# Kernel optimization log

Measured on AMD Instinct MI355X. Metric: run time of the kernel, lower is better.

## Reference

```python
import jax, jax.numpy as jnp
import numpy as np

DIM = 512
K = 64          # num_clusters
GHOST = 1
ALPHA = 100.0
EPS = 1e-12


def _l2norm(v, axis):
    return v / jnp.maximum(jnp.linalg.norm(v, axis=axis, keepdims=True), EPS)


def setup_inputs() -> dict:
    key = jax.random.key(0)
    k_x, k_c = jax.random.split(key)
    x = jax.random.normal(k_x, (64, DIM, 32, 32), dtype=jnp.float32)
    # centroids ~ orthogonal init in torch; random normal rows, unit-ish scale
    centroids = jax.random.normal(k_c, (K + GHOST, DIM), dtype=jnp.float32) / np.sqrt(DIM)
    conv_w = 2.0 * ALPHA * centroids            # [K+g, C] (1x1 conv kernel squeezed)
    conv_b = -ALPHA * jnp.linalg.norm(centroids, axis=1)  # [K+g]
    return {"x": x, "centroids": centroids, "conv_w": conv_w, "conv_b": conv_b}


def reference(x, centroids, conv_w, conv_b):
    N, C, H, W = x.shape
    L = H * W
    # descriptor-wise L2 normalization over channel dim
    xn = _l2norm(x, axis=1)
    xf = xn.reshape(N, C, L)                                   # [N, C, L]
    # 1x1 conv == per-location matmul; softmax over clusters
    logits = jnp.einsum('kc,ncl->nkl', conv_w, xf) + conv_b[None, :, None]
    a = jax.nn.softmax(logits, axis=1)                         # [N, K+g, L]
    # vlad[n,k,c] = sum_l a[n,k,l]*(x[n,c,l]-cent[k,c])
    #            = (a @ x^T) - (sum_l a) * cent   -- avoids NxKxCxL tensor
    weighted = jnp.einsum('nkl,ncl->nkc', a, xf)               # [N, K+g, C]
    a_sum = jnp.sum(a, axis=-1)                                # [N, K+g]
    vlad = weighted - a_sum[:, :, None] * centroids[None]      # [N, K+g, C]
    vlad = vlad[:, :K, :]                                      # drop ghost clusters
    vlad = _l2norm(vlad, axis=2)                               # intra-normalization
    vlad = vlad.reshape(N, K * C)
    vlad = _l2norm(vlad, axis=1)                               # global L2
    return vlad
```

## Files before the change

kernel.cpp:

```cpp
#include <hip/hip_runtime.h>
#include <hip/hip_bf16.h>

#define C_DIM 512
#define L_DIM 1024
#define KK 64
#define KG 65
#define KP 80

using f32x4  = __attribute__((ext_vector_type(4))) float;
using bf16x8 = __attribute__((ext_vector_type(8))) short;

union U4 { uint4 u; bf16x8 b; };

__device__ __forceinline__ unsigned bfh(float x) { return __float_as_uint(x) >> 16; }
__device__ __forceinline__ float bfh_f(float x) { return __uint_as_float(__float_as_uint(x) & 0xFFFF0000u); }

__device__ __forceinline__ unsigned pack2(float a, float b) {
    return __builtin_amdgcn_perm(__float_as_uint(b), __float_as_uint(a), 0x07060302u);
}

__device__ __forceinline__ void load_lds16(const void* g, void* l) {
    __builtin_amdgcn_global_load_lds(
        (const __attribute__((address_space(1))) void*)g,
        (__attribute__((address_space(3))) void*)l, 16, 0, 0);
}

__global__ void k_prep(const float* __restrict__ conv_w, const float* __restrict__ conv_b,
                       unsigned short* __restrict__ wp, float* __restrict__ wb)
{
    int ch = blockIdx.x;
    int kt = blockIdx.y;
    int t  = threadIdx.x;
    for (int p = 0; p < 2; ++p) {
        int idx = p * 256 + t;
        int lane = idx >> 3, j = idx & 7;
        int k = kt * 16 + (lane & 15);
        int c = ch * 32 + (lane >> 4) * 8 + j;
        float v = (k < KG) ? conv_w[k * C_DIM + c] : 0.f;
        unsigned h = bfh(v);
        float r = v - __uint_as_float(h << 16);
        wp[((ch * 10 + kt) << 9) + idx]     = (unsigned short)h;
        wp[((ch * 10 + 5 + kt) << 9) + idx] = (unsigned short)bfh(r);
    }
    if (ch == 0 && kt == 0 && t < KP) wb[t] = (t < KG) ? conv_b[t] : -1e30f;
}

__global__ __launch_bounds__(256) void k_s1(
    const float* __restrict__ x, const unsigned short* __restrict__ wp,
    const float* __restrict__ wb,
    unsigned* __restrict__ aPh32, unsigned* __restrict__ aPl32,
    float* __restrict__ asum_part)
{
    __shared__ unsigned short wlds[2][10 << 9];

    const int lb = blockIdx.x, n = blockIdx.y;
    const int t = threadIdx.x, lane = t & 63, w = t >> 6;
    const int arow = lane & 15;
    const int agrp = lane >> 4;
    const int lw0 = lb * 128 + w * 32;
    const int choff = (lb + n) & 15;

    const float* xbase = x + (size_t)n * C_DIM * L_DIM;

#define WSTAGE(b, ch) { _Pragma("unroll") \
    for (int i = 0; i < 3; ++i) { \
        int s = w + (i << 2); \
        if (s < 10) { \
            const unsigned short* src = &wp[(((ch) * 10 + s) << 9) + (lane << 3)]; \
            load_lds16(src, &wlds[b][s << 9]); \
        } } }

    f32x4 acc[5][2];
#pragma unroll
    for (int a = 0; a < 5; ++a)
#pragma unroll
        for (int b = 0; b < 2; ++b) acc[a][b] = (f32x4)0.f;
    float ss0 = 0.f, ss1 = 0.f;

    WSTAGE(0, choff)
    asm volatile("s_waitcnt vmcnt(0)" ::: "memory");
    __syncthreads();

#pragma unroll 2
    for (int ch0 = 0; ch0 < 16; ++ch0) {
        const int cur = ch0 & 1;
        const int ch = (ch0 + choff) & 15;
        const int c0 = ch * 32;
        if (ch0 < 15) WSTAGE(cur ^ 1, (ch0 + 1 + choff) & 15)
        float e0[8], e1[8];
#pragma unroll
        for (int j = 0; j < 8; ++j) {
            float2 v = *reinterpret_cast<const float2*>(
                &xbase[(size_t)(c0 + agrp * 8 + j) * L_DIM + lw0 + 2 * arow]);
            e0[j] = v.x;
            e1[j] = v.y;
        }
#pragma unroll
        for (int j = 0; j < 8; ++j) { ss0 += e0[j] * e0[j]; ss1 += e1[j] * e1[j]; }
        U4 bh[2], bl[2];
        bh[0].u.x = pack2(e0[0], e0[1]); bh[0].u.y = pack2(e0[2], e0[3]);
        bh[0].u.z = pack2(e0[4], e0[5]); bh[0].u.w = pack2(e0[6], e0[7]);
        bh[1].u.x = pack2(e1[0], e1[1]); bh[1].u.y = pack2(e1[2], e1[3]);
        bh[1].u.z = pack2(e1[4], e1[5]); bh[1].u.w = pack2(e1[6], e1[7]);
        float r0, r1, r2, r3;
        r0 = e0[0] - bfh_f(e0[0]); r1 = e0[1] - bfh_f(e0[1]);
        r2 = e0[2] - bfh_f(e0[2]); r3 = e0[3] - bfh_f(e0[3]);
        bl[0].u.x = pack2(r0, r1); bl[0].u.y = pack2(r2, r3);
        r0 = e0[4] - bfh_f(e0[4]); r1 = e0[5] - bfh_f(e0[5]);
        r2 = e0[6] - bfh_f(e0[6]); r3 = e0[7] - bfh_f(e0[7]);
        bl[0].u.z = pack2(r0, r1); bl[0].u.w = pack2(r2, r3);
        r0 = e1[0] - bfh_f(e1[0]); r1 = e1[1] - bfh_f(e1[1]);
        r2 = e1[2] - bfh_f(e1[2]); r3 = e1[3] - bfh_f(e1[3]);
        bl[1].u.x = pack2(r0, r1); bl[1].u.y = pack2(r2, r3);
        r0 = e1[4] - bfh_f(e1[4]); r1 = e1[5] - bfh_f(e1[5]);
        r2 = e1[6] - bfh_f(e1[6]); r3 = e1[7] - bfh_f(e1[7]);
        bl[1].u.z = pack2(r0, r1); bl[1].u.w = pack2(r2, r3);
        U4 ah[5], al[5];
#pragma unroll
        for (int kt = 0; kt < 5; ++kt) {
            ah[kt].u = *reinterpret_cast<const uint4*>(&wlds[cur][(kt << 9) + (lane << 3)]);
            al[kt].u = *reinterpret_cast<const uint4*>(&wlds[cur][((5 + kt) << 9) + (lane << 3)]);
        }
#pragma unroll
        for (int kt = 0; kt < 5; ++kt)
#pragma unroll
            for (int lt = 0; lt < 2; ++lt) {
                acc[kt][lt] = __builtin_amdgcn_mfma_f32_16x16x32_bf16(ah[kt].b, bh[lt].b, acc[kt][lt], 0, 0, 0);
                acc[kt][lt] = __builtin_amdgcn_mfma_f32_16x16x32_bf16(ah[kt].b, bl[lt].b, acc[kt][lt], 0, 0, 0);
                acc[kt][lt] = __builtin_amdgcn_mfma_f32_16x16x32_bf16(al[kt].b, bh[lt].b, acc[kt][lt], 0, 0, 0);
            }
        asm volatile("s_waitcnt vmcnt(0)" ::: "memory");
        __syncthreads();
    }

    ss0 += __shfl_xor(ss0, 16, 64); ss0 += __shfl_xor(ss0, 32, 64);
    ss1 += __shfl_xor(ss1, 16, 64); ss1 += __shfl_xor(ss1, 32, 64);
    float invc[2];
    invc[0] = 1.0f / fmaxf(sqrtf(ss0), 1e-12f);
    invc[1] = 1.0f / fmaxf(sqrtf(ss1), 1e-12f);

    float4 wbv[5];
#pragma unroll
    for (int kt = 0; kt < 5; ++kt)
        wbv[kt] = *reinterpret_cast<const float4*>(&wb[kt * 16 + agrp * 4]);

    float aval[5][2][4];
    float rs[2];
#pragma unroll
    for (int lt = 0; lt < 2; ++lt) {
        float m = -1e30f;
#pragma unroll
        for (int kt = 0; kt < 5; ++kt)
#pragma unroll
            for (int r = 0; r < 4; ++r) {
                float lg = acc[kt][lt][r] * invc[lt] + ((const float*)&wbv[kt])[r];
                aval[kt][lt][r] = lg;
                m = fmaxf(m, lg);
            }
        m = fmaxf(m, __shfl_xor(m, 16, 64));
        m = fmaxf(m, __shfl_xor(m, 32, 64));
        float s = 0.f;
#pragma unroll
        for (int kt = 0; kt < 5; ++kt)
#pragma unroll
            for (int r = 0; r < 4; ++r) {
                float e = __expf(aval[kt][lt][r] - m);
                aval[kt][lt][r] = e;
                s += e;
            }
        s += __shfl_xor(s, 16, 64);
        s += __shfl_xor(s, 32, 64);
        rs[lt] = 1.0f / s;
    }

#pragma unroll
    for (int kt = 0; kt < 4; ++kt)
#pragma unroll
        for (int r = 0; r < 4; ++r) {
            int k = kt * 16 + agrp * 4 + r;
            float s01 = 0.f;
#pragma unroll
            for (int lt = 0; lt < 2; ++lt) {
                float a = aval[kt][lt][r] * rs[lt];
                aval[kt][lt][r] = a;
                s01 += a;
            }
#pragma unroll
            for (int off = 8; off; off >>= 1) s01 += __shfl_xor(s01, off, 64);
            if ((lane & 15) == 0)
                asum_part[((n * 8 + lb) * 4 + w) * KK + k] = s01;
            float ap0 = aval[kt][0][r] * invc[0];
            float ap1 = aval[kt][1][r] * invc[1];
            unsigned h0 = bfh(ap0), h1 = bfh(ap1);
            float q0 = ap0 - __uint_as_float(h0 << 16);
            float q1 = ap1 - __uint_as_float(h1 << 16);
            int widx = (n * KK + k) * (L_DIM / 2) + (lw0 >> 1) + arow;
            aPh32[widx] = h0 | (h1 << 16);
            aPl32[widx] = bfh(q0) | (bfh(q1) << 16);
        }
}

__global__ void k_asum(const float* __restrict__ part, float* __restrict__ a_sum)
{
    int id = blockIdx.x * 256 + threadIdx.x;
    int n = id >> 6, k = id & 63;
    float s = 0.f;
#pragma unroll
    for (int p = 0; p < 32; ++p) s += part[(n * 32 + p) * KK + k];
    a_sum[id] = s;
}

#define S2P 72
__global__ __launch_bounds__(256) void k_s2v(
    const float* __restrict__ x, const unsigned short* __restrict__ aPh,
    const unsigned short* __restrict__ aPl, const float* __restrict__ a_sum,
    const float* __restrict__ cent, float* __restrict__ vlad,
    float* __restrict__ rnpart)
{
    __shared__ unsigned short Ah[64 * S2P], Al[64 * S2P];
    __shared__ unsigned short Bh[64 * S2P], Bl[64 * S2P];
    __shared__ float rnbuf[4][64];

    const int flat = blockIdx.x;
    const int cq = flat >> 6;
    const int n  = ((flat & 7) << 3) | ((flat >> 3) & 7);
    const int t = threadIdx.x, lane = t & 63, w = t >> 6;
    const int arow = lane & 15, agrp = lane >> 4;

    f32x4 acc[4];
#pragma unroll
    for (int a = 0; a < 4; ++a) acc[a] = (f32x4)0.f;

    for (int step = 0; step < 16; ++step) {
        const int l0 = step * 64;
        __syncthreads();
#pragma unroll
        for (int p = 0; p < 2; ++p) {
            int idx = p * 256 + t;
            int k = idx >> 3;
            int lc = (idx & 7) * 8;
            size_t g = (size_t)(n * KK + k) * L_DIM + l0 + lc;
            *reinterpret_cast<uint4*>(&Ah[k * S2P + lc]) = *reinterpret_cast<const uint4*>(&aPh[g]);
            *reinterpret_cast<uint4*>(&Al[k * S2P + lc]) = *reinterpret_cast<const uint4*>(&aPl[g]);
        }
#pragma unroll
        for (int p = 0; p < 4; ++p) {
            int idx = p * 256 + t;
            int c = idx >> 4;
            int lc = (idx & 15) * 4;
            float4 v = *reinterpret_cast<const float4*>(
                &x[((size_t)n * C_DIM + cq * 64 + c) * L_DIM + l0 + lc]);
            uint2 hw, lw;
            hw.x = pack2(v.x, v.y); hw.y = pack2(v.z, v.w);
            float r0 = v.x - bfh_f(v.x), r1 = v.y - bfh_f(v.y);
            float r2 = v.z - bfh_f(v.z), r3 = v.w - bfh_f(v.w);
            lw.x = pack2(r0, r1); lw.y = pack2(r2, r3);
            *reinterpret_cast<uint2*>(&Bh[c * S2P + lc]) = hw;
            *reinterpret_cast<uint2*>(&Bl[c * S2P + lc]) = lw;
        }
        __syncthreads();
#pragma unroll
        for (int ks = 0; ks < 2; ++ks) {
            const int koff = ks * 32 + agrp * 8;
            U4 bh, bl;
            bh.u = *reinterpret_cast<const uint4*>(&Bh[(w * 16 + arow) * S2P + koff]);
            bl.u = *reinterpret_cast<const uint4*>(&Bl[(w * 16 + arow) * S2P + koff]);
#pragma unroll
            for (int kt = 0; kt < 4; ++kt) {
                U4 ah, al;
                ah.u = *reinterpret_cast<const uint4*>(&Ah[(kt * 16 + arow) * S2P + koff]);
                al.u = *reinterpret_cast<const uint4*>(&Al[(kt * 16 + arow) * S2P + koff]);
                acc[kt] = __builtin_amdgcn_mfma_f32_16x16x32_bf16(ah.b, bh.b, acc[kt], 0, 0, 0);
                acc[kt] = __builtin_amdgcn_mfma_f32_16x16x32_bf16(ah.b, bl.b, acc[kt], 0, 0, 0);
                acc[kt] = __builtin_amdgcn_mfma_f32_16x16x32_bf16(al.b, bh.b, acc[kt], 0, 0, 0);
            }
        }
    }
    const int c = cq * 64 + w * 16 + arow;
    float myrn[4][4];
#pragma unroll
    for (int kt = 0; kt < 4; ++kt)
#pragma unroll
        for (int r = 0; r < 4; ++r) {
            int k = kt * 16 + agrp * 4 + r;
            float as = a_sum[n * 64 + k];
            float cv = cent[k * C_DIM + c];
            float v = acc[kt][r] - as * cv;
            vlad[((size_t)n * KK + k) * C_DIM + c] = v;
            float sq = v * v;
            sq += __shfl_xor(sq, 1, 64);
            sq += __shfl_xor(sq, 2, 64);
            sq += __shfl_xor(sq, 4, 64);
            sq += __shfl_xor(sq, 8, 64);
            myrn[kt][r] = sq;
        }
    if (arow == 0) {
#pragma unroll
        for (int kt = 0; kt < 4; ++kt)
#pragma unroll
            for (int r = 0; r < 4; ++r)
                rnbuf[w][kt * 16 + agrp * 4 + r] = myrn[kt][r];
    }
    __syncthreads();
    if (t < 64) {
        float s = rnbuf[0][t] + rnbuf[1][t] + rnbuf[2][t] + rnbuf[3][t];
        rnpart[((size_t)n * 64 + t) * 8 + cq] = s;
    }
}

__global__ void k_scale(const float* __restrict__ rnpart, float* __restrict__ scale)
{
    int n = blockIdx.x;
    int k = threadIdx.x;
    float s = 0.f;
#pragma unroll
    for (int q = 0; q < 8; ++q) s += rnpart[((size_t)n * 64 + k) * 8 + q];
    float nrm = sqrtf(s);
    float den = fmaxf(nrm, 1e-12f);
    float tk = nrm / den;
    float tot = tk * tk;
#pragma unroll
    for (int off = 32; off; off >>= 1) tot += __shfl_down(tot, off, 64);
    tot = __shfl(tot, 0, 64);
    float g = fmaxf(sqrtf(tot), 1e-12f);
    scale[n * 64 + k] = 1.0f / (den * g);
}

__global__ void k_out(const float* __restrict__ vlad, const float* __restrict__ scale,
                      float* __restrict__ out)
{
    int nk = blockIdx.x;
    int t = threadIdx.x;
    float sc = scale[nk];
    for (int c = t; c < C_DIM; c += 256)
        out[(size_t)nk * C_DIM + c] = vlad[(size_t)nk * C_DIM + c] * sc;
}

extern "C" void kernel_launch(void* const* d_in, const int* in_sizes, int n_in,
                              void* d_out, int out_size, void* d_ws, size_t ws_size,
                              hipStream_t stream)
{
    const float* x    = (const float*)d_in[0];
    const float* cent = (const float*)d_in[1];
    const float* cw   = (const float*)d_in[2];
    const float* cb   = (const float*)d_in[3];
    float* out = (float*)d_out;
    char* ws = (char*)d_ws;

    unsigned short* wp  = (unsigned short*)(ws + 0);
    float*          wb  = (float*)(ws + 262144);
    unsigned short* aPh = (unsigned short*)(ws + 524288);
    unsigned short* aPl = (unsigned short*)(ws + 8912896);
    float* asum_part    = (float*)(ws + 17301504);
    float* a_sum        = (float*)(ws + 17825792);
    float* vlad         = (float*)(ws + 18874368);
    float* rnpart       = (float*)(ws + 27262976);
    float* scale        = (float*)(ws + 27394048);

    k_prep<<<dim3(16, 5), 256, 0, stream>>>(cw, cb, wp, wb);
    k_s1<<<dim3(8, 64), 256, 0, stream>>>(x, wp, wb,
                                          (unsigned*)aPh, (unsigned*)aPl, asum_part);
    k_asum<<<16, 256, 0, stream>>>(asum_part, a_sum);
    k_s2v<<<512, 256, 0, stream>>>(x, aPh, aPl, a_sum, cent, vlad, rnpart);
    k_scale<<<64, 64, 0, stream>>>(rnpart, scale);
    k_out<<<4096, 256, 0, stream>>>(vlad, scale, out);
}
```

Baseline: 74.44 us.

## Stage x tiles through LDS with async two-deep prefetch and counted waits

Activation tiles are now loaded with global_load_lds into a double-buffered, padded LDS array alongside the weight tiles, prefetching two channel chunks ahead. The full vmcnt(0) drain at the end of each iteration is replaced by per-wave counted waits (vmcnt 6 or 7) followed by a barrier, so the next chunk's loads stay in flight during MFMA work. This targets the exposed global-load latency of the strided float2 x reads in the main loop. In exchange it uses more LDS, which may lower occupancy, and relies on exact per-wave load counts for correctness.

```diff
diff --git a/kernel.cpp b/kernel.cpp
--- a/kernel.cpp
+++ b/kernel.cpp
@@ -45,30 +45,39 @@
     if (ch == 0 && kt == 0 && t < KP) wb[t] = (t < KG) ? conv_b[t] : -1e30f;
 }
 
+#define XSEG 260
 __global__ __launch_bounds__(256) void k_s1(
     const float* __restrict__ x, const unsigned short* __restrict__ wp,
     const float* __restrict__ wb,
     unsigned* __restrict__ aPh32, unsigned* __restrict__ aPl32,
     float* __restrict__ asum_part)
 {
+    __shared__ float xs[2][16 * XSEG];
     __shared__ unsigned short wlds[2][10 << 9];
 
     const int lb = blockIdx.x, n = blockIdx.y;
     const int t = threadIdx.x, lane = t & 63, w = t >> 6;
     const int arow = lane & 15;
     const int agrp = lane >> 4;
-    const int lw0 = lb * 128 + w * 32;
+    const int gl0 = lb * 128;
+    const int lw0 = gl0 + w * 32;
     const int choff = (lb + n) & 15;
 
     const float* xbase = x + (size_t)n * C_DIM * L_DIM;
 
-#define WSTAGE(b, ch) { _Pragma("unroll") \
-    for (int i = 0; i < 3; ++i) { \
-        int s = w + (i << 2); \
-        if (s < 10) { \
-            const unsigned short* src = &wp[(((ch) * 10 + s) << 9) + (lane << 3)]; \
-            load_lds16(src, &wlds[b][s << 9]); \
-        } } }
+#define XSTAGE(b, ch) { _Pragma("unroll") \
+    for (int i = 0; i < 4; ++i) { \
+        int s = w * 4 + i; \
+        const float* src = &xbase[(size_t)((ch) * 32 + s * 2 + (lane >> 5)) * L_DIM \
+                                  + gl0 + (lane & 31) * 4]; \
+        load_lds16(src, &xs[b][s * XSEG]); \
+    } }
+#define WSTAGE(b, ch) { \
+    load_lds16(&wp[(((ch) * 10 + w) << 9) + (lane << 3)], &wlds[b][w << 9]); \
+    load_lds16(&wp[(((ch) * 10 + w + 4) << 9) + (lane << 3)], &wlds[b][(w + 4) << 9]); \
+    if (w < 2) \
+        load_lds16(&wp[(((ch) * 10 + 8 + w) << 9) + (lane << 3)], &wlds[b][(8 + w) << 9]); \
+    }
 
     f32x4 acc[5][2];
 #pragma unroll
@@ -77,21 +86,24 @@
         for (int b = 0; b < 2; ++b) acc[a][b] = (f32x4)0.f;
     float ss0 = 0.f, ss1 = 0.f;
 
-    WSTAGE(0, choff)
-    asm volatile("s_waitcnt vmcnt(0)" ::: "memory");
-    __syncthreads();
+    XSTAGE(0, choff) WSTAGE(0, choff)
+    XSTAGE(1, (1 + choff) & 15) WSTAGE(1, (1 + choff) & 15)
 
 #pragma unroll 2
     for (int ch0 = 0; ch0 < 16; ++ch0) {
         const int cur = ch0 & 1;
         const int ch = (ch0 + choff) & 15;
-        const int c0 = ch * 32;
-        if (ch0 < 15) WSTAGE(cur ^ 1, (ch0 + 1 + choff) & 15)
+        if (ch0 == 15) { asm volatile("s_waitcnt vmcnt(0)" ::: "memory"); }
+        else if (w < 2) { asm volatile("s_waitcnt vmcnt(7)" ::: "memory"); }
+        else            { asm volatile("s_waitcnt vmcnt(6)" ::: "memory"); }
+        __builtin_amdgcn_s_barrier();
+        __builtin_amdgcn_sched_barrier(0);
         float e0[8], e1[8];
 #pragma unroll
         for (int j = 0; j < 8; ++j) {
+            int c = agrp * 8 + j;
             float2 v = *reinterpret_cast<const float2*>(
-                &xbase[(size_t)(c0 + agrp * 8 + j) * L_DIM + lw0 + 2 * arow]);
+                &xs[cur][(c >> 1) * XSEG + (c & 1) * 128 + w * 32 + 2 * arow]);
             e0[j] = v.x;
             e1[j] = v.y;
         }
@@ -129,8 +141,11 @@
                 acc[kt][lt] = __builtin_amdgcn_mfma_f32_16x16x32_bf16(ah[kt].b, bl[lt].b, acc[kt][lt], 0, 0, 0);
                 acc[kt][lt] = __builtin_amdgcn_mfma_f32_16x16x32_bf16(al[kt].b, bh[lt].b, acc[kt][lt], 0, 0, 0);
             }
-        asm volatile("s_waitcnt vmcnt(0)" ::: "memory");
-        __syncthreads();
+        __builtin_amdgcn_s_barrier();
+        if (ch0 < 14) {
+            const int nx = (ch0 + 2 + choff) & 15;
+            XSTAGE(cur, nx) WSTAGE(cur, nx)
+        }
     }
 
     ss0 += __shfl_xor(ss0, 16, 64); ss0 += __shfl_xor(ss0, 32, 64);
```

Result: faster. 71.09 us (median of 2 runs) (-4.5%).
